# Performance work log

Hardware: AMD Instinct MI355X
Metric: run time of the kernel (lower is better)

Reference implementation:

```python
import jax, jax.numpy as jnp
import numpy as np
import itertools

D_MODEL = 1024
TEMP = 0.3


def _hypercube(n):
    # all 2^n corners of {-1,+1}^n, matching generate_hypercube(n)
    return jnp.asarray(np.array(list(itertools.product([-1.0, 1.0], repeat=n)), dtype=np.float32))


def setup_inputs() -> dict:
    key = jax.random.key(0)
    ks = jax.random.split(key, 12)
    B, T, D = 8, 4096, D_MODEL
    s = 0.02
    return {
        "x": jax.random.normal(ks[0], (B, T, D), dtype=jnp.float32),
        "codes_l1": _hypercube(3),   # (8, 3)
        "codes_l2": _hypercube(6),   # (64, 6)
        "w_to_l1": jax.random.normal(ks[1], (D, 3), dtype=jnp.float32) * s,
        "w_from_l1": jax.random.normal(ks[2], (3, D), dtype=jnp.float32) * s,
        "w_to_l2": jax.random.normal(ks[3], (D, 6), dtype=jnp.float32) * s,
        "w_from_l2": jax.random.normal(ks[4], (6, D), dtype=jnp.float32) * s,
        "w_to_l3u": jax.random.normal(ks[5], (D, 6), dtype=jnp.float32) * s,
        "w_to_l3l": jax.random.normal(ks[6], (D, 6), dtype=jnp.float32) * s,
        "w_from_l3": jax.random.normal(ks[7], (12, D), dtype=jnp.float32) * s,
        "w_gate": jax.random.normal(ks[8], (D, 3), dtype=jnp.float32) * s,
        "b_gate": jnp.zeros((3,), dtype=jnp.float32),
        "temp_l1": jnp.log(jnp.float32(TEMP)),
        "temp_l2": jnp.log(jnp.float32(TEMP * 0.7)),
        "temp_l3": jnp.log(jnp.float32(TEMP * 0.5)),
        "scale_l1": jnp.float32(0.1),
        "scale_l2": jnp.float32(0.05),
        "scale_l3": jnp.float32(0.02),
    }


def _soft_quantize(z, codes, temp_log):
    # z: (B, T, n); codes: (K, n) -> (B, T, n)
    temp = jnp.clip(jnp.exp(temp_log), 0.01, 5.0)
    # Euclidean cdist: (B, T, K)
    dists = jnp.sqrt(jnp.sum(jnp.square(z[..., None, :] - codes), axis=-1))
    weights = jax.nn.softmax(-dists / temp, axis=-1)
    return weights @ codes


def reference(x, codes_l1, codes_l2, w_to_l1, w_from_l1, w_to_l2, w_from_l2,
              w_to_l3u, w_to_l3l, w_from_l3, w_gate, b_gate,
              temp_l1, temp_l2, temp_l3, scale_l1, scale_l2, scale_l3):
    # gate uses detached x
    gate = jax.nn.softmax(jax.lax.stop_gradient(x) @ w_gate + b_gate, axis=-1)  # (B,T,3)

    # Level 1: Z2^3
    q1 = _soft_quantize(x @ w_to_l1, codes_l1, temp_l1)
    out_l1 = q1 @ w_from_l1

    # Level 2: Z2^6
    q2 = _soft_quantize(x @ w_to_l2, codes_l2, temp_l2)
    out_l2 = q2 @ w_from_l2

    # Level 3: Z2^12 = two Z2^6 halves
    q3u = _soft_quantize(x @ w_to_l3u, codes_l2, temp_l3)
    q3l = _soft_quantize(x @ w_to_l3l, codes_l2, temp_l3)
    out_l3 = jnp.concatenate([q3u, q3l], axis=-1) @ w_from_l3

    out = (gate[..., 0:1] * scale_l1 * out_l1
           + gate[..., 1:2] * scale_l2 * out_l2
           + gate[..., 2:3] * scale_l3 * out_l3)
    gate_means = jnp.mean(gate, axis=(0, 1))  # stats dict analogue: (3,)
    return x + out, gate_means
```

## Files before the change

kernel.cpp:

```cpp
#include <hip/hip_runtime.h>
#include <stdint.h>


#define DM 1024
#define TPB 64
#define OUT_OFF ((size_t)33554432)
#define NTOK 32768
#define NSLOT 32
#define WSA_OFF 32768

typedef float f32x4 __attribute__((ext_vector_type(4)));
typedef short bf16x8 __attribute__((ext_vector_type(8)));

typedef const __attribute__((address_space(1))) unsigned int* gas1_t;
typedef __attribute__((address_space(3))) unsigned int* las3_t;

__device__ __forceinline__ void gl_lds16(const void* g, void* l){
  __builtin_amdgcn_global_load_lds((gas1_t)g, (las3_t)l, 16, 0, 0);
}

__device__ __forceinline__ short f2bf(float f){
  unsigned u = __builtin_bit_cast(unsigned, f);
  unsigned r = u + 0x7fffu + ((u >> 16) & 1u);
  return (short)(r >> 16);
}

template<int NB>
__device__ __forceinline__ void softq(const float* z, float invt, float* q){
  constexpr int K = 1 << NB;
  float d[K];
  float dmin = 3.4e38f;
#pragma unroll
  for (int j = 0; j < K; ++j){
    float acc = 0.f;
#pragma unroll
    for (int i = 0; i < NB; ++i){
      float c = ((j >> (NB-1-i)) & 1) ? 1.f : -1.f;
      float t = z[i] - c;
      acc = fmaf(t, t, acc);
    }
    float dj = sqrtf(acc);
    d[j] = dj;
    dmin = fminf(dmin, dj);
  }
  float S = 0.f;
  float s1[NB];
#pragma unroll
  for (int i = 0; i < NB; ++i) s1[i] = 0.f;
#pragma unroll
  for (int j = 0; j < K; ++j){
    float wj = __expf((dmin - d[j]) * invt);
    S += wj;
#pragma unroll
    for (int i = 0; i < NB; ++i)
      if ((j >> (NB-1-i)) & 1) s1[i] += wj;
  }
  float rS = 1.f / S;
#pragma unroll
  for (int i = 0; i < NB; ++i) q[i] = 2.f * s1[i] * rS - 1.f;
}

__global__ __launch_bounds__(256) void pack_kernel(
    const float* __restrict__ w_to_l1,  const float* __restrict__ w_to_l2,
    const float* __restrict__ w_to_l3u, const float* __restrict__ w_to_l3l,
    const float* __restrict__ w_gate,
    const float* __restrict__ w_from_l1, const float* __restrict__ w_from_l2,
    const float* __restrict__ w_from_l3,
    short* __restrict__ wsF, float* __restrict__ wsA)
{
  int base = blockIdx.x*4096 + threadIdx.x*16;
#pragma unroll
  for (int q = 0; q < 16; ++q){
    int e = base + q;
    float v;
    if (e < 32768){
      int s  = e >> 10;
      int nf = (e >> 9) & 1;
      int ll = (e >> 3) & 63;
      int j  = e & 7;
      int k  = s*32 + ((ll >> 4) << 3) + j;
      int n  = nf*16 + (ll & 15);
      if      (n < 3)  v = w_gate  [k*3 + n];
      else if (n < 6)  v = w_to_l1 [k*3 + (n-3)];
      else if (n < 12) v = w_to_l2 [k*6 + (n-6)];
      else if (n < 18) v = w_to_l3u[k*6 + (n-12)];
      else if (n < 24) v = w_to_l3l[k*6 + (n-18)];
      else             v = 0.f;
    } else {
      int e2  = e - 32768;
      int f   = e2 / 384;
      int rem = e2 - f*384;
      int ll  = rem >> 3;
      int j   = e2 & 7;
      int k   = ((ll >> 4) << 3) + j;
      int dd  = f*16 + (ll & 15);
      if      (k < 3)  v = w_from_l1[k*DM + dd];
      else if (k < 9)  v = w_from_l2[(k-3)*DM + dd];
      else if (k < 21) v = w_from_l3[(k-9)*DM + dd];
      else             v = 0.f;
    }
    wsF[e] = f2bf(v);
  }
  if (blockIdx.x == 0){
    wsA[threadIdx.x]       = 0.f;
    wsA[threadIdx.x + 256] = 0.f;
  }
}

__global__ __launch_bounds__(256, 2) void hq5_kernel(
    const float* __restrict__ x, const short* __restrict__ wsF,
    const float* __restrict__ b_gate,
    const float* __restrict__ t1p, const float* __restrict__ t2p, const float* __restrict__ t3p,
    const float* __restrict__ s1p, const float* __restrict__ s2p, const float* __restrict__ s3p,
    float* __restrict__ wsA, float* __restrict__ out)
{
  __shared__ alignas(16) char smem[79808];
  float* C   = reinterpret_cast<float*>(smem + 32768);
  float* P   = reinterpret_cast<float*>(smem + 65536);
  short* V16 = reinterpret_cast<short*>(smem + 74496);
  float* GS  = reinterpret_cast<float*>(smem + 79616);

  const int tid  = threadIdx.x;
  const int l    = tid & 63;
  const int wv   = tid >> 6;
  const int kg   = l >> 4;
  const int ln16 = l & 15;
  const int tb   = blockIdx.x * TPB;

  f32x4 acc0 = {0.f,0.f,0.f,0.f}, acc1 = {0.f,0.f,0.f,0.f};
  {
    const int lr0 = l >> 5;
    const int cbp = l & 31;
#pragma unroll
    for (int i = 0; i < 8; ++i){
      int lr = i*2 + lr0;
      gl_lds16(x + (size_t)(tb + wv*16 + lr)*DM + (cbp ^ (lr & 7))*4,
               smem + wv*16384 + i*1024 + l*16);
    }
#pragma unroll
    for (int t = 0; t < 8; ++t){
      const int buf = t & 1;
      bf16x8 bfr[8];
#pragma unroll
      for (int s2 = 0; s2 < 8; ++s2)
        bfr[s2] = *reinterpret_cast<const bf16x8*>(&wsF[(t*8 + s2)*512 + l*8]);
      __builtin_amdgcn_sched_barrier(0);
      if (t < 7){
#pragma unroll
        for (int i = 0; i < 8; ++i){
          int lr = i*2 + lr0;
          gl_lds16(x + (size_t)(tb + wv*16 + lr)*DM + (t+1)*128 + (cbp ^ (lr & 7))*4,
                   smem + wv*16384 + (buf^1)*8192 + i*1024 + l*16);
        }
        asm volatile("s_waitcnt vmcnt(8)" ::: "memory");
      } else {
        asm volatile("s_waitcnt vmcnt(0)" ::: "memory");
      }
      const char* abase = smem + wv*16384 + buf*8192 + ln16*512;
#pragma unroll
      for (int s = 0; s < 4; ++s){
        float4 xa = *reinterpret_cast<const float4*>(abase + ((s*8 + kg*2 + 0) ^ (ln16 & 7))*16);
        float4 xb = *reinterpret_cast<const float4*>(abase + ((s*8 + kg*2 + 1) ^ (ln16 & 7))*16);
        bf16x8 af;
        af[0]=f2bf(xa.x); af[1]=f2bf(xa.y); af[2]=f2bf(xa.z); af[3]=f2bf(xa.w);
        af[4]=f2bf(xb.x); af[5]=f2bf(xb.y); af[6]=f2bf(xb.z); af[7]=f2bf(xb.w);
        acc0 = __builtin_amdgcn_mfma_f32_16x16x32_bf16(af, bfr[s*2+0], acc0, 0, 0, 0);
        acc1 = __builtin_amdgcn_mfma_f32_16x16x32_bf16(af, bfr[s*2+1], acc1, 0, 0, 0);
      }
    }
#pragma unroll
    for (int r = 0; r < 4; ++r){
      int row = wv*16 + kg*4 + r;
      P[row*35 + ln16]      = acc0[r];
      P[row*35 + 16 + ln16] = acc1[r];
    }
  }
  __syncthreads();

  {
#pragma unroll
    for (int j = 0; j < 4; ++j){
      int lr = j*4 + (l >> 4);
      gl_lds16(x + (size_t)(tb + wv*16 + lr)*DM + ((l & 15) ^ (lr & 7))*4,
               smem + wv*8192 + j*1024 + l*16);
    }
  }

  float qv[6] = {0,0,0,0,0,0};
  float myscale = 0.f;
  {
    const int t = l;
    const int base = (wv == 3) ? 0 : 6 + wv*6;
    float z[6];
#pragma unroll
    for (int i = 0; i < 6; ++i) z[i] = P[t*35 + base + i];
    if (wv == 3){
      float invt1 = 1.f / fminf(fmaxf(__expf(t1p[0]), 0.01f), 5.0f);
      float g0l = z[0] + b_gate[0];
      float g1l = z[1] + b_gate[1];
      float g2l = z[2] + b_gate[2];
      float m  = fmaxf(g0l, fmaxf(g1l, g2l));
      float e0 = __expf(g0l - m), e1 = __expf(g1l - m), e2 = __expf(g2l - m);
      float rs = 1.f / (e0 + e1 + e2);
      float g0 = e0*rs, g1 = e1*rs, g2 = e2*rs;
      GS[t*3+0] = g0 * s1p[0];
      GS[t*3+1] = g1 * s2p[0];
      GS[t*3+2] = g2 * s3p[0];
      myscale   = g0 * s1p[0];
      float z1[3] = {z[3], z[4], z[5]};
      softq<3>(z1, invt1, qv);
      float sg0=g0, sg1=g1, sg2=g2;
#pragma unroll
      for (int mm = 1; mm < 64; mm <<= 1){
        sg0 += __shfl_xor(sg0, mm, 64);
        sg1 += __shfl_xor(sg1, mm, 64);
        sg2 += __shfl_xor(sg2, mm, 64);
      }
      if (t == 0){
        float* slot = wsA + (blockIdx.x & (NSLOT-1))*16;
        atomicAdd(slot + 0, sg0);
        atomicAdd(slot + 1, sg1);
        atomicAdd(slot + 2, sg2);
      }
    } else {
      float tl = (wv == 0) ? t2p[0] : t3p[0];
      float invt = 1.f / fminf(fmaxf(__expf(tl), 0.01f), 5.0f);
      softq<6>(z, invt, qv);
    }
  }
  __syncthreads();

  {
    const int t = l;
    if (wv == 3){
#pragma unroll
      for (int i = 0; i < 3; ++i) V16[t*40 + i] = f2bf(myscale * qv[i]);
      V16[t*40 + 21] = 0; V16[t*40 + 22] = 0; V16[t*40 + 23] = 0;
    } else {
      float sc = GS[t*3 + ((wv == 0) ? 1 : 2)];
      int voff = 3 + wv*6;
#pragma unroll
      for (int i = 0; i < 6; ++i) V16[t*40 + voff + i] = f2bf(sc * qv[i]);
    }
  }
  __syncthreads();

  bf16x8 aV = {0,0,0,0,0,0,0,0};
  if (kg < 3)
    aV = *reinterpret_cast<const bf16x8*>(&V16[(wv*16 + ln16)*40 + kg*8]);
  const short* wsFC = wsF + 32768;
  const f32x4 z4 = {0.f,0.f,0.f,0.f};
  const int rl = l >> 2;
  const int cs = l & 3;

#pragma unroll
  for (int c = 0; c < 16; ++c){
    const int buf = c & 1;
    bf16x8 bw[4];
#pragma unroll
    for (int ff = 0; ff < 4; ++ff){
      bw[ff] = (bf16x8){0,0,0,0,0,0,0,0};
      if (kg < 3)
        bw[ff] = *reinterpret_cast<const bf16x8*>(&wsFC[(c*4+ff)*384 + l*8]);
    }
    __builtin_amdgcn_sched_barrier(0);
    if (c < 15){
#pragma unroll
      for (int j = 0; j < 4; ++j){
        int lr = j*4 + (l >> 4);
        gl_lds16(x + (size_t)(tb + wv*16 + lr)*DM + (c+1)*64 + (((l & 15) ^ (lr & 7)))*4,
                 smem + wv*8192 + (buf^1)*4096 + j*1024 + l*16);
      }
      asm volatile("s_waitcnt vmcnt(4)" ::: "memory");
    } else {
      asm volatile("s_waitcnt vmcnt(0)" ::: "memory");
    }
#pragma unroll
    for (int ff = 0; ff < 4; ++ff){
      f32x4 dd = __builtin_amdgcn_mfma_f32_16x16x32_bf16(aV, bw[ff], z4, 0, 0, 0);
#pragma unroll
      for (int r = 0; r < 4; ++r)
        C[(wv*16 + kg*4 + r)*68 + ff*16 + ln16] = dd[r];
    }
    asm volatile("s_waitcnt lgkmcnt(0)" ::: "memory");
    __builtin_amdgcn_sched_barrier(0);
#pragma unroll
    for (int q = 0; q < 4; ++q){
      int bi = cs + 4*q;
      float4 xv = *reinterpret_cast<const float4*>(
          smem + wv*8192 + buf*4096 + rl*256 + ((bi ^ (rl & 7)))*16);
      float4 cv = *reinterpret_cast<const float4*>(&C[(wv*16 + rl)*68 + bi*4]);
      float4 ov = {xv.x+cv.x, xv.y+cv.y, xv.z+cv.z, xv.w+cv.w};
      *reinterpret_cast<float4*>(
          &out[(size_t)(tb + wv*16 + rl)*DM + c*64 + bi*4]) = ov;
    }
  }
}

__global__ void finalize_kernel(const float* __restrict__ wsA, float* __restrict__ out){
  if (threadIdx.x < 3){
    float s = 0.f;
    for (int j = 0; j < NSLOT; ++j) s += wsA[j*16 + threadIdx.x];
    out[OUT_OFF + threadIdx.x] = s * (1.f / (float)NTOK);
  }
}

extern "C" void kernel_launch(void* const* d_in, const int* in_sizes, int n_in,
                              void* d_out, int out_size, void* d_ws, size_t ws_size,
                              hipStream_t stream){
  (void)in_sizes; (void)n_in; (void)ws_size; (void)out_size;
  const float* x         = (const float*)d_in[0];
  const float* w_to_l1   = (const float*)d_in[3];
  const float* w_from_l1 = (const float*)d_in[4];
  const float* w_to_l2   = (const float*)d_in[5];
  const float* w_from_l2 = (const float*)d_in[6];
  const float* w_to_l3u  = (const float*)d_in[7];
  const float* w_to_l3l  = (const float*)d_in[8];
  const float* w_from_l3 = (const float*)d_in[9];
  const float* w_gate    = (const float*)d_in[10];
  const float* b_gate    = (const float*)d_in[11];
  const float* t1 = (const float*)d_in[12];
  const float* t2 = (const float*)d_in[13];
  const float* t3 = (const float*)d_in[14];
  const float* s1 = (const float*)d_in[15];
  const float* s2 = (const float*)d_in[16];
  const float* s3 = (const float*)d_in[17];
  float* out  = (float*)d_out;
  short* wsF  = (short*)d_ws;
  float* wsA  = (float*)d_ws + WSA_OFF;

  pack_kernel<<<dim3(14), dim3(256), 0, stream>>>(
      w_to_l1, w_to_l2, w_to_l3u, w_to_l3l, w_gate,
      w_from_l1, w_from_l2, w_from_l3, wsF, wsA);
  hq5_kernel<<<dim3(512), dim3(256), 0, stream>>>(
      x, wsF, b_gate, t1, t2, t3, s1, s2, s3, wsA, out);
  finalize_kernel<<<dim3(1), dim3(64), 0, stream>>>(wsA, out);
}
```

Baseline: 80.83 us.

## Triple-buffer output-phase x loads and prefetch weight fragments one chunk ahead

The output phase now uses a three-deep LDS ring for x chunks, prefetching two chunks ahead instead of one. It also loads the next chunk's from-weights into registers during the current iteration. Output stores become nontemporal, and the gate-mean atomics move to the end of the kernel. The aim is to hide global load latency in the memory-bound residual-add loop and avoid polluting cache with output writes. In exchange the kernel uses more LDS, carries more registers and relies on hand-tuned vmcnt waits.

Result: slower. 90.93 us (+12.5%).

```diff
diff --git a/kernel.cpp b/kernel.cpp
--- a/kernel.cpp
+++ b/kernel.cpp
@@ -107,18 +107,18 @@
   }
 }
 
-__global__ __launch_bounds__(256, 2) void hq5_kernel(
+__global__ __launch_bounds__(256, 2) void hq6_kernel(
     const float* __restrict__ x, const short* __restrict__ wsF,
     const float* __restrict__ b_gate,
     const float* __restrict__ t1p, const float* __restrict__ t2p, const float* __restrict__ t3p,
     const float* __restrict__ s1p, const float* __restrict__ s2p, const float* __restrict__ s3p,
     float* __restrict__ wsA, float* __restrict__ out)
 {
-  __shared__ alignas(16) char smem[79808];
-  float* C   = reinterpret_cast<float*>(smem + 32768);
-  float* P   = reinterpret_cast<float*>(smem + 65536);
-  short* V16 = reinterpret_cast<short*>(smem + 74496);
-  float* GS  = reinterpret_cast<float*>(smem + 79616);
+  __shared__ alignas(16) char smem[80576];
+  float* C   = reinterpret_cast<float*>(smem + 49152);
+  float* P   = reinterpret_cast<float*>(smem + 66560);
+  short* V16 = reinterpret_cast<short*>(smem + 75264);
+  float* GS  = reinterpret_cast<float*>(smem + 80384);
 
   const int tid  = threadIdx.x;
   const int l    = tid & 63;
@@ -127,8 +127,8 @@
   const int ln16 = l & 15;
   const int tb   = blockIdx.x * TPB;
 
-  f32x4 acc0 = {0.f,0.f,0.f,0.f}, acc1 = {0.f,0.f,0.f,0.f};
   {
+    f32x4 acc0 = {0.f,0.f,0.f,0.f}, acc1 = {0.f,0.f,0.f,0.f};
     const int lr0 = l >> 5;
     const int cbp = l & 31;
 #pragma unroll
@@ -171,29 +171,44 @@
 #pragma unroll
     for (int r = 0; r < 4; ++r){
       int row = wv*16 + kg*4 + r;
-      P[row*35 + ln16]      = acc0[r];
-      P[row*35 + 16 + ln16] = acc1[r];
+      P[row*34 + ln16]      = acc0[r];
+      P[row*34 + 16 + ln16] = acc1[r];
     }
   }
   __syncthreads();
 
+  const short* wsFC = wsF + 32768;
+  bf16x8 bwc0={0,0,0,0,0,0,0,0}, bwc1=bwc0, bwc2=bwc0, bwc3=bwc0;
   {
 #pragma unroll
     for (int j = 0; j < 4; ++j){
       int lr = j*4 + (l >> 4);
       gl_lds16(x + (size_t)(tb + wv*16 + lr)*DM + ((l & 15) ^ (lr & 7))*4,
-               smem + wv*8192 + j*1024 + l*16);
+               smem + wv*12288 + j*1024 + l*16);
+    }
+    if (kg < 3){
+      bwc0 = *reinterpret_cast<const bf16x8*>(&wsFC[(0*4+0)*384 + l*8]);
+      bwc1 = *reinterpret_cast<const bf16x8*>(&wsFC[(0*4+1)*384 + l*8]);
+      bwc2 = *reinterpret_cast<const bf16x8*>(&wsFC[(0*4+2)*384 + l*8]);
+      bwc3 = *reinterpret_cast<const bf16x8*>(&wsFC[(0*4+3)*384 + l*8]);
+    }
+#pragma unroll
+    for (int j = 0; j < 4; ++j){
+      int lr = j*4 + (l >> 4);
+      gl_lds16(x + (size_t)(tb + wv*16 + lr)*DM + 64 + ((l & 15) ^ (lr & 7))*4,
+               smem + wv*12288 + 4096 + j*1024 + l*16);
     }
   }
 
   float qv[6] = {0,0,0,0,0,0};
   float myscale = 0.f;
+  float sg0 = 0.f, sg1 = 0.f, sg2 = 0.f;
   {
     const int t = l;
     const int base = (wv == 3) ? 0 : 6 + wv*6;
     float z[6];
 #pragma unroll
-    for (int i = 0; i < 6; ++i) z[i] = P[t*35 + base + i];
+    for (int i = 0; i < 6; ++i) z[i] = P[t*34 + base + i];
     if (wv == 3){
       float invt1 = 1.f / fminf(fmaxf(__expf(t1p[0]), 0.01f), 5.0f);
       float g0l = z[0] + b_gate[0];
@@ -209,18 +224,12 @@
       myscale   = g0 * s1p[0];
       float z1[3] = {z[3], z[4], z[5]};
       softq<3>(z1, invt1, qv);
-      float sg0=g0, sg1=g1, sg2=g2;
+      sg0 = g0; sg1 = g1; sg2 = g2;
 #pragma unroll
       for (int mm = 1; mm < 64; mm <<= 1){
         sg0 += __shfl_xor(sg0, mm, 64);
         sg1 += __shfl_xor(sg1, mm, 64);
         sg2 += __shfl_xor(sg2, mm, 64);
-      }
-      if (t == 0){
-        float* slot = wsA + (blockIdx.x & (NSLOT-1))*16;
-        atomicAdd(slot + 0, sg0);
-        atomicAdd(slot + 1, sg1);
-        atomicAdd(slot + 2, sg2);
       }
     } else {
       float tl = (wv == 0) ? t2p[0] : t3p[0];
@@ -248,52 +257,67 @@
   bf16x8 aV = {0,0,0,0,0,0,0,0};
   if (kg < 3)
     aV = *reinterpret_cast<const bf16x8*>(&V16[(wv*16 + ln16)*40 + kg*8]);
-  const short* wsFC = wsF + 32768;
   const f32x4 z4 = {0.f,0.f,0.f,0.f};
   const int rl = l >> 2;
   const int cs = l & 3;
 
 #pragma unroll
   for (int c = 0; c < 16; ++c){
-    const int buf = c & 1;
-    bf16x8 bw[4];
-#pragma unroll
-    for (int ff = 0; ff < 4; ++ff){
-      bw[ff] = (bf16x8){0,0,0,0,0,0,0,0};
-      if (kg < 3)
-        bw[ff] = *reinterpret_cast<const bf16x8*>(&wsFC[(c*4+ff)*384 + l*8]);
-    }
-    __builtin_amdgcn_sched_barrier(0);
-    if (c < 15){
+    if (c == 0 || c == 15) asm volatile("s_waitcnt vmcnt(4)" ::: "memory");
+    else                   asm volatile("s_waitcnt vmcnt(8)" ::: "memory");
+    __builtin_amdgcn_sched_barrier(0);
+    {
+      f32x4 d0 = __builtin_amdgcn_mfma_f32_16x16x32_bf16(aV, bwc0, z4, 0, 0, 0);
+      f32x4 d1 = __builtin_amdgcn_mfma_f32_16x16x32_bf16(aV, bwc1, z4, 0, 0, 0);
+      f32x4 d2 = __builtin_amdgcn_mfma_f32_16x16x32_bf16(aV, bwc2, z4, 0, 0, 0);
+      f32x4 d3 = __builtin_amdgcn_mfma_f32_16x16x32_bf16(aV, bwc3, z4, 0, 0, 0);
+#pragma unroll
+      for (int r = 0; r < 4; ++r){
+        int rowb = (wv*16 + kg*4 + r)*68;
+        C[rowb +  0 + ln16] = d0[r];
+        C[rowb + 16 + ln16] = d1[r];
+        C[rowb + 32 + ln16] = d2[r];
+        C[rowb + 48 + ln16] = d3[r];
+      }
+    }
+    __builtin_amdgcn_sched_barrier(0);
+    bf16x8 bwn0 = bwc0, bwn1 = bwc1, bwn2 = bwc2, bwn3 = bwc3;
+    if (c < 15 && kg < 3){
+      bwn0 = *reinterpret_cast<const bf16x8*>(&wsFC[((c+1)*4+0)*384 + l*8]);
+      bwn1 = *reinterpret_cast<const bf16x8*>(&wsFC[((c+1)*4+1)*384 + l*8]);
+      bwn2 = *reinterpret_cast<const bf16x8*>(&wsFC[((c+1)*4+2)*384 + l*8]);
+      bwn3 = *reinterpret_cast<const bf16x8*>(&wsFC[((c+1)*4+3)*384 + l*8]);
+    }
+    __builtin_amdgcn_sched_barrier(0);
+    if (c < 14){
 #pragma unroll
       for (int j = 0; j < 4; ++j){
         int lr = j*4 + (l >> 4);
-        gl_lds16(x + (size_t)(tb + wv*16 + lr)*DM + (c+1)*64 + (((l & 15) ^ (lr & 7)))*4,
-                 smem + wv*8192 + (buf^1)*4096 + j*1024 + l*16);
-      }
-      asm volatile("s_waitcnt vmcnt(4)" ::: "memory");
-    } else {
-      asm volatile("s_waitcnt vmcnt(0)" ::: "memory");
-    }
-#pragma unroll
-    for (int ff = 0; ff < 4; ++ff){
-      f32x4 dd = __builtin_amdgcn_mfma_f32_16x16x32_bf16(aV, bw[ff], z4, 0, 0, 0);
-#pragma unroll
-      for (int r = 0; r < 4; ++r)
-        C[(wv*16 + kg*4 + r)*68 + ff*16 + ln16] = dd[r];
-    }
+        gl_lds16(x + (size_t)(tb + wv*16 + lr)*DM + (c+2)*64 + ((l & 15) ^ (lr & 7))*4,
+                 smem + wv*12288 + ((c+2)%3)*4096 + j*1024 + l*16);
+      }
+    }
+    __builtin_amdgcn_sched_barrier(0);
     asm volatile("s_waitcnt lgkmcnt(0)" ::: "memory");
     __builtin_amdgcn_sched_barrier(0);
 #pragma unroll
     for (int q = 0; q < 4; ++q){
       int bi = cs + 4*q;
-      float4 xv = *reinterpret_cast<const float4*>(
-          smem + wv*8192 + buf*4096 + rl*256 + ((bi ^ (rl & 7)))*16);
-      float4 cv = *reinterpret_cast<const float4*>(&C[(wv*16 + rl)*68 + bi*4]);
-      float4 ov = {xv.x+cv.x, xv.y+cv.y, xv.z+cv.z, xv.w+cv.w};
-      *reinterpret_cast<float4*>(
-          &out[(size_t)(tb + wv*16 + rl)*DM + c*64 + bi*4]) = ov;
-    }
+      f32x4 xv = *reinterpret_cast<const f32x4*>(
+          smem + wv*12288 + (c%3)*4096 + rl*256 + ((bi ^ (rl & 7)))*16);
+      f32x4 cv = *reinterpret_cast<const f32x4*>(&C[(wv*16 + rl)*68 + bi*4]);
+      f32x4 ov = xv + cv;
+      __builtin_nontemporal_store(ov,
+          reinterpret_cast<f32x4*>(&out[(size_t)(tb + wv*16 + rl)*DM + c*64 + bi*4]));
+    }
+    bwc0 = bwn0; bwc1 = bwn1; bwc2 = bwn2; bwc3 = bwn3;
+  }
+
+  if (wv == 3 && l == 0){
+    float* slot = wsA + (blockIdx.x & (NSLOT-1))*16;
+    atomicAdd(slot + 0, sg0);
+    atomicAdd(slot + 1, sg1);
+    atomicAdd(slot + 2, sg2);
   }
 }
 
@@ -332,7 +356,7 @@
   pack_kernel<<<dim3(14), dim3(256), 0, stream>>>(
       w_to_l1, w_to_l2, w_to_l3u, w_to_l3l, w_gate,
       w_from_l1, w_from_l2, w_from_l3, wsF, wsA);
-  hq5_kernel<<<dim3(512), dim3(256), 0, stream>>>(
+  hq6_kernel<<<dim3(512), dim3(256), 0, stream>>>(
       x, wsF, b_gate, t1, t2, t3, s1, s2, s3, wsA, out);
   finalize_kernel<<<dim3(1), dim3(64), 0, stream>>>(wsA, out);
 }
```
